# Kernel tuning notes

Measured on AMD Instinct MI355X. Metric: run time of the kernel, lower is better.

Reference implementation:

```python
import jax, jax.numpy as jnp
import numpy as np

S, H, W_GRID, F, B = 256, 256, 256, 6, 4096


def setup_inputs() -> dict:
    key = jax.random.key(0)
    k1, k2, k3, k4 = jax.random.split(key, 4)
    feats = jax.random.normal(k1, (B, 2, F), dtype=jnp.float32)
    # coordinate channels 6..9 hold integer grid indices stored as floats
    coords = jax.random.randint(k2, (B, 2, 4), 0, H).astype(jnp.float32)
    phi = jnp.concatenate([feats, coords], axis=-1)            # [B, 2, 10]
    w_lin = jax.random.normal(k3, (1, F), dtype=jnp.float32) * 0.1
    succ_feats = jax.random.normal(k4, (S, H, W_GRID, F), dtype=jnp.float32)
    return {"phi": phi, "w_lin": w_lin, "succ_feats": succ_feats}


def _get_vals(succ_feats, w_lin, xs, ys):
    # xs, ys: [B, 2] int32 grid coordinates
    sel = succ_feats[:, xs, ys]                 # [S, B, 2, F] gather
    sel = jnp.transpose(sel, (1, 0, 2, 3))      # [B, S, 2, F]
    vs = jnp.einsum('bstf,of->bsto', sel, w_lin)  # [B, S, 2, 1]
    p = jax.nn.softmax(vs, axis=1)              # softmax over S states
    return jnp.sum(p * vs, axis=1)[..., 0]      # [B, 2]


def reference(phi, w_lin, succ_feats):
    pr = jnp.einsum('btf,of->bto', phi[:, :, 0:F], w_lin)[..., 0]  # [B, 2]
    ss_x = phi[:, :, 6].astype(jnp.int32)
    ss_y = phi[:, :, 7].astype(jnp.int32)
    es_x = phi[:, :, 8].astype(jnp.int32)
    es_y = phi[:, :, 9].astype(jnp.int32)
    # get_vals runs under torch.no_grad() in the original -> stop_gradient
    v_ss = jax.lax.stop_gradient(_get_vals(succ_feats, w_lin, ss_x, ss_y))
    v_es = jax.lax.stop_gradient(_get_vals(succ_feats, w_lin, es_x, es_y))
    left_der = pr[:, 0:1] + (v_es[:, 0:1] - v_ss[:, 0:1])   # [B, 1]
    right_der = pr[:, 1:2] + (v_es[:, 1:2] - v_ss[:, 1:2])  # [B, 1]
    left_pred = jax.nn.sigmoid(left_der - right_der)
    right_pred = jax.nn.sigmoid(right_der - left_der)
    return jnp.stack([left_pred, right_pred], axis=1)        # [B, 2, 1]
```

## Files before the change

kernel.cpp:

```cpp
#include <hip/hip_runtime.h>
#include <math.h>

#define S_DIM 256
#define H_DIM 256
#define W_DIM 256
#define F_DIM 6
#define B_DIM 4096
#define NCELL (H_DIM * W_DIM)
#define SLICE ((size_t)NCELL * F_DIM)


__global__ __launch_bounds__(512) void build_vtable_dense(const float* __restrict__ succ,
                                                          const float* __restrict__ w_lin,
                                                          float* __restrict__ V) {
    __shared__ float4 acc[8][64];

    const int tid = threadIdx.x;
    const int ch  = tid >> 6;
    const int pr  = tid & 63;
    const int c0  = blockIdx.x * 128;

    const float w0 = w_lin[0], w1 = w_lin[1], w2 = w_lin[2],
                w3 = w_lin[3], w4 = w_lin[4], w5 = w_lin[5];

    const float* p = succ + (size_t)(ch * 32) * SLICE
                          + (size_t)(c0 + 2 * pr) * F_DIM;

    float l0 = 0.f, n0 = 0.f, l1 = 0.f, n1 = 0.f;
    #pragma unroll 4
    for (int i = 0; i < 32; ++i) {
        float4 a = ((const float4*)p)[0];
        float4 b = ((const float4*)p)[1];
        float4 d = ((const float4*)p)[2];
        p += SLICE;
        float vA = a.x*w0 + a.y*w1 + a.z*w2 + a.w*w3 + b.x*w4 + b.y*w5;
        float vB = b.z*w0 + b.w*w1 + d.x*w2 + d.y*w3 + d.z*w4 + d.w*w5;
        float eA = __expf(vA);
        float eB = __expf(vB);
        l0 += eA; n0 = fmaf(eA, vA, n0);
        l1 += eB; n1 = fmaf(eB, vB, n1);
    }
    acc[ch][pr] = make_float4(l0, n0, l1, n1);
    __syncthreads();

    if (tid < 128) {
        const int pair = tid >> 1;
        const int odd  = tid & 1;
        float L = 0.f, N = 0.f;
        #pragma unroll
        for (int k = 0; k < 8; ++k) {
            float4 t = acc[k][pair];
            L += odd ? t.z : t.x;
            N += odd ? t.w : t.y;
        }
        V[c0 + tid] = N / L;
    }
}

__global__ void eval_queries(const float* __restrict__ phi,
                             const float* __restrict__ w_lin,
                             const float* __restrict__ V,
                             float* __restrict__ out) {
    const int b = blockIdx.x * blockDim.x + threadIdx.x;
    if (b >= B_DIM) return;

    const float w0 = w_lin[0], w1 = w_lin[1], w2 = w_lin[2],
                w3 = w_lin[3], w4 = w_lin[4], w5 = w_lin[5];

    const float* p = phi + (size_t)b * 20;
    float der[2];
    #pragma unroll
    for (int t = 0; t < 2; ++t) {
        const float* q = p + t * 10;
        float pr = q[0]*w0 + q[1]*w1 + q[2]*w2 + q[3]*w3 + q[4]*w4 + q[5]*w5;
        int ssx = (int)q[6];
        int ssy = (int)q[7];
        int esx = (int)q[8];
        int esy = (int)q[9];
        float v_ss = V[ssx * 256 + ssy];
        float v_es = V[esx * 256 + esy];
        der[t] = pr + (v_es - v_ss);
    }
    float d = der[0] - der[1];
    out[b * 2 + 0] = 1.f / (1.f + __expf(-d));
    out[b * 2 + 1] = 1.f / (1.f + __expf(d));
}

extern "C" void kernel_launch(void* const* d_in, const int* in_sizes, int n_in,
                              void* d_out, int out_size, void* d_ws, size_t ws_size,
                              hipStream_t stream) {
    const float* phi   = (const float*)d_in[0];
    const float* w_lin = (const float*)d_in[1];
    const float* succ  = (const float*)d_in[2];
    float* out = (float*)d_out;

    float* V = (float*)d_ws;

    build_vtable_dense<<<512, 512, 0, stream>>>(succ, w_lin, V);
    eval_queries<<<(B_DIM + 255) / 256, 256, 0, stream>>>(phi, w_lin, V, out);
}
```

Measured before the change: 525.3 us.

## Restructure vtable build to 256 blocks with two S-halves per block

Reworks the dense value-table kernel so each block of 256 threads covers 128 cell pairs and splits the 256 states into two halves of 128 iterations each, instead of 512 blocks of 512 threads with 8 state chunks. The two partial softmax sums are then combined and written as one float2 per thread. The aim is fewer blocks, less shared-memory reduction work and a longer streaming loop per thread. The risk is lower occupancy and fewer loads in flight on a kernel bound by memory bandwidth, since the grid drops to 256 blocks.

```diff
diff --git a/kernel.cpp b/kernel.cpp
--- a/kernel.cpp
+++ b/kernel.cpp
@@ -10,25 +10,25 @@
 #define SLICE ((size_t)NCELL * F_DIM)
 
 
-__global__ __launch_bounds__(512) void build_vtable_dense(const float* __restrict__ succ,
-                                                          const float* __restrict__ w_lin,
-                                                          float* __restrict__ V) {
-    __shared__ float4 acc[8][64];
+__global__ __launch_bounds__(256) void build_vtable_linear(const float* __restrict__ succ,
+                                                           const float* __restrict__ w_lin,
+                                                           float* __restrict__ V) {
+    __shared__ float4 acc[256];
 
-    const int tid = threadIdx.x;
-    const int ch  = tid >> 6;
-    const int pr  = tid & 63;
-    const int c0  = blockIdx.x * 128;
+    const int tid   = threadIdx.x;
+    const int lane  = tid & 127;
+    const int shalf = tid >> 7;
+    const int pairG = blockIdx.x * 128 + lane;
 
     const float w0 = w_lin[0], w1 = w_lin[1], w2 = w_lin[2],
                 w3 = w_lin[3], w4 = w_lin[4], w5 = w_lin[5];
 
-    const float* p = succ + (size_t)(ch * 32) * SLICE
-                          + (size_t)(c0 + 2 * pr) * F_DIM;
+    const float* p = succ + (size_t)(shalf * 128) * SLICE
+                          + (size_t)pairG * (2 * F_DIM);
 
     float l0 = 0.f, n0 = 0.f, l1 = 0.f, n1 = 0.f;
-    #pragma unroll 4
-    for (int i = 0; i < 32; ++i) {
+    #pragma unroll 8
+    for (int i = 0; i < 128; ++i) {
         float4 a = ((const float4*)p)[0];
         float4 b = ((const float4*)p)[1];
         float4 d = ((const float4*)p)[2];
@@ -40,20 +40,16 @@
         l0 += eA; n0 = fmaf(eA, vA, n0);
         l1 += eB; n1 = fmaf(eB, vB, n1);
     }
-    acc[ch][pr] = make_float4(l0, n0, l1, n1);
+    acc[tid] = make_float4(l0, n0, l1, n1);
     __syncthreads();
 
     if (tid < 128) {
-        const int pair = tid >> 1;
-        const int odd  = tid & 1;
-        float L = 0.f, N = 0.f;
-        #pragma unroll
-        for (int k = 0; k < 8; ++k) {
-            float4 t = acc[k][pair];
-            L += odd ? t.z : t.x;
-            N += odd ? t.w : t.y;
-        }
-        V[c0 + tid] = N / L;
+        float4 A = acc[tid];
+        float4 Bv = acc[tid + 128];
+        float2 r;
+        r.x = (A.y + Bv.y) / (A.x + Bv.x);
+        r.y = (A.w + Bv.w) / (A.z + Bv.z);
+        *(float2*)&V[2 * pairG] = r;
     }
 }
 
@@ -96,6 +92,6 @@
 
     float* V = (float*)d_ws;
 
-    build_vtable_dense<<<512, 512, 0, stream>>>(succ, w_lin, V);
+    build_vtable_linear<<<256, 256, 0, stream>>>(succ, w_lin, V);
     eval_queries<<<(B_DIM + 255) / 256, 256, 0, stream>>>(phi, w_lin, V, out);
 }
```

After: 522.8 us. Within noise of the previous version (-0.5%).
